# Performance work log

Measured on AMD Instinct MI355X. Metric: run time of the kernel, lower is better.

## Reference

```python
import math
import jax, jax.numpy as jnp
import numpy as np

B, D, COND, H, K, L, BOUND = 262144, 16, 8, 128, 10, 4, 1.0
D2 = math.ceil(D / 2)          # second split (spline-transformed channels) = 8
D1 = D - D2                    # passthrough channels = 8
DOUT = (3 * K + 1) * D2        # subnet output = 248
PMIN = 1e-3                    # BIN_WIDTH_MIN == BIN_HEIGHT_MIN == DELTA_MIN


def setup_inputs() -> dict:
    key = jax.random.key(0)
    ks = jax.random.split(key, 8)
    x = jax.random.normal(ks[0], (B, D), dtype=jnp.float32)
    c = jax.random.normal(ks[1], (B, COND), dtype=jnp.float32)
    din1 = D1 + COND
    W1s = jax.random.normal(ks[2], (L, din1, H), dtype=jnp.float32) * 0.1
    b1s = jnp.zeros((L, H), dtype=jnp.float32)
    Whs = jax.random.normal(ks[3], (L, H, H), dtype=jnp.float32) * 0.1
    bhs = jnp.zeros((L, H), dtype=jnp.float32)
    Wos = jax.random.normal(ks[4], (L, H, DOUT), dtype=jnp.float32) * 0.1
    bos = jnp.zeros((L, DOUT), dtype=jnp.float32)
    rng = np.random.default_rng(0)  # permutation_seed = 0
    perms = jnp.asarray(np.stack([rng.permutation(D) for _ in range(L)]), dtype=jnp.int32)
    return {"x": x, "c": c, "W1s": W1s, "b1s": b1s, "Whs": Whs, "bhs": bhs,
            "Wos": Wos, "bos": bos, "perms": perms}


def _softmax_with_min(t, m):
    return m + (1.0 - m * t.shape[-1]) * jax.nn.softmax(t, axis=-1)


def _unpack_theta(theta):
    # theta: [B, D2, 3K+1]
    bw_u, bh_u, ks_u = theta[..., :K], theta[..., K:2 * K], theta[..., 2 * K:]
    bin_w = 2.0 * BOUND * _softmax_with_min(bw_u, PMIN)
    bin_h = 2.0 * BOUND * _softmax_with_min(bh_u, PMIN)
    slopes = PMIN + (1.0 - PMIN) * jax.nn.softplus(ks_u) / math.log(2.0)
    pad = ((0, 0), (0, 0), (1, 0))
    x_knots = jnp.pad(jnp.cumsum(bin_w, axis=-1), pad) - BOUND
    y_knots = jnp.pad(jnp.cumsum(bin_h, axis=-1), pad) - BOUND
    return x_knots, y_knots, bin_w, bin_h, slopes


def _spline_fwd(x2, x_knots, y_knots, bin_w, bin_h, slopes):
    # x2: [B, D2]; knots: [B, D2, K+1]; widths/heights: [B, D2, K]; slopes: [B, D2, K+1]
    bin_idx = jnp.sum(x_knots < x2[..., None], axis=-1) - 1  # searchsorted(left) - 1
    in_bounds = (bin_idx >= 0) & (bin_idx < K)
    ci = jnp.clip(bin_idx, 0, K - 1)
    g = lambda t, i: jnp.take_along_axis(t, i[..., None], axis=-1)[..., 0]
    x1, y1 = g(x_knots, ci), g(y_knots, ci)
    xw, yw = g(bin_w, ci), g(bin_h, ci)
    d1, d2 = g(slopes, ci), g(slopes, ci + 1)
    # safe x so rational-quadratic never produces nan for masked-out lanes
    xs = jnp.where(in_bounds, x2, x1 + 0.5 * xw)
    s = yw / xw
    eta = (xs - x1) / xw
    rev_eta = 1.0 - eta
    err = eta * rev_eta
    y_denom = s + (d1 + d2 - 2.0 * s) * err
    y_rq = y1 + yw * (s * eta ** 2 + d1 * err) / y_denom
    jac_num = s ** 2 * (d2 * eta ** 2 + 2.0 * s * err + d1 * rev_eta ** 2)
    log_jac = jnp.log(jac_num) - 2.0 * jnp.log(y_denom)
    # out-of-bounds: linear extrapolation through the outermost knots
    xl, xr = x_knots[..., 0], x_knots[..., -1]
    yb, yt = y_knots[..., 0], y_knots[..., -1]
    y_lin = (yt - yb) / (xr - xl) * (x2 - xl) + yb
    yx = jnp.where(in_bounds, y_rq, y_lin)
    log_jac = jnp.where(in_bounds, log_jac, 0.0)
    return yx, jnp.sum(log_jac, axis=-1)


def _flow_forward(x, c, W1s, b1s, Whs, bhs, Wos, bos, perms):
    log_jac_det = jnp.zeros((x.shape[0],), dtype=x.dtype)
    for i in range(L):
        x1, x2 = x[:, :D1], x[:, D1:]
        h = jax.nn.relu(jnp.concatenate([x1, c], axis=1) @ W1s[i] + b1s[i])
        h = jax.nn.relu(h @ Whs[i] + bhs[i])
        theta = (h @ Wos[i] + bos[i]).reshape(-1, D2, 3 * K + 1)
        x_knots, y_knots, bin_w, bin_h, slopes = _unpack_theta(theta)
        y2, ljd = _spline_fwd(x2, x_knots, y_knots, bin_w, bin_h, slopes)
        log_jac_det = log_jac_det + ljd
        x_out = jnp.concatenate([x1, y2], axis=1)
        x = jnp.take(x_out, perms[i], axis=1)  # x @ channel_perm.T
    return x, log_jac_det


def reference(x, c, W1s, b1s, Whs, bhs, Wos, bos, perms):
    return _flow_forward(x, c, W1s, b1s, Whs, bhs, Wos, bos, perms)
```

## Files before the change

kernel.cpp:

```cpp
#include <hip/hip_runtime.h>

#define B_N   262144
#define PMIN_F 0.001f
#define LOG2E 1.44269504088896340736f
#define LN2   0.69314718055994530942f

typedef _Float16 half4v __attribute__((ext_vector_type(4)));
typedef _Float16 half8  __attribute__((ext_vector_type(8)));
typedef float    floatx4 __attribute__((ext_vector_type(4)));

__device__ __forceinline__ float fexp2(float x) { return __builtin_amdgcn_exp2f(x); }
__device__ __forceinline__ float flog2(float x) { return __builtin_amdgcn_logf(x); }
__device__ __forceinline__ float frcp (float x) { return __builtin_amdgcn_rcpf(x); }

__global__ __launch_bounds__(64) void prep_kernel(
    const float* __restrict__ W1s, const float* __restrict__ b1s,
    const float* __restrict__ Whs, const float* __restrict__ Wos,
    _Float16* __restrict__ ws)
{
    const int bid   = blockIdx.x;
    const int layer = bid / 104;
    const int r     = bid % 104;
    const int lane  = threadIdx.x;
    const int kg    = lane >> 4;
    const int c     = lane & 15;

    half8 v;
    if (r < 8) {
        const int nt = r, n = nt * 16 + c;
        const float* W1 = W1s + layer * 16 * 128;
        const float* b1 = b1s + layer * 128;
        #pragma unroll
        for (int j = 0; j < 8; ++j) {
            const int k = kg * 8 + j;
            v[j] = (k < 16) ? (_Float16)W1[k * 128 + n]
                 : (k == 16) ? (_Float16)b1[n] : (_Float16)0.f;
        }
    } else if (r < 40) {
        const int f = r - 8, nt = f >> 2, ks = f & 3, n = nt * 16 + c;
        const float* Wh = Whs + layer * 128 * 128;
        #pragma unroll
        for (int j = 0; j < 8; ++j) {
            const int k = ks * 32 + kg * 8 + j;
            v[j] = (_Float16)Wh[k * 128 + n];
        }
    } else {
        const int f = r - 40, nt = f >> 2, ks = f & 3, n = nt * 16 + c;
        const int dd = n >> 5, cc = n & 31;
        const float* Wo = Wos + layer * 128 * 248;
        #pragma unroll
        for (int j = 0; j < 8; ++j) {
            const int k = ks * 32 + kg * 8 + j;
            v[j] = (cc < 31) ? (_Float16)Wo[k * 248 + dd * 31 + cc] : (_Float16)0.f;
        }
    }
    *(half8*)(ws + (size_t)bid * 512 + lane * 8) = v;
}

__global__ __launch_bounds__(64) void flow_mfma(
    const float* __restrict__ x_in,
    const float* __restrict__ c_in,
    const float* __restrict__ bhs,
    const float* __restrict__ bos,
    const int*   __restrict__ perms,
    const _Float16* __restrict__ wsW,
    float* __restrict__ out)
{
    __shared__ __align__(16) float    xls[2][256];
    __shared__ __align__(16) _Float16 cls[2][128];
    __shared__ __align__(16) _Float16 R[2][4224];

    const int lane = threadIdx.x;
    const int q    = lane >> 4;
    const int m    = lane & 15;
    const long long row0 = (long long)blockIdx.x * 32;

    {
        const float4* xp = (const float4*)(x_in + row0 * 16);
        *(float4*)&xls[0][lane * 4] = xp[lane];
        *(float4*)&xls[1][lane * 4] = xp[lane + 64];
        const float2* cp = (const float2*)(c_in + row0 * 8);
        const float2 c0 = cp[lane], c1 = cp[lane + 64];
        cls[0][lane * 2]     = (_Float16)c0.x;
        cls[0][lane * 2 + 1] = (_Float16)c0.y;
        cls[1][lane * 2]     = (_Float16)c1.x;
        cls[1][lane * 2 + 1] = (_Float16)c1.y;
    }
    __syncthreads();

    float ljacc[4] = {0.f, 0.f, 0.f, 0.f};

    for (int l = 0; l < 4; ++l) {
        const _Float16* wsl = wsW + (size_t)l * 104 * 512;
        const float* bh = bhs + l * 128;
        const float* bo = bos + l * 248;

        half8 a1[2];
        #pragma unroll
        for (int t2 = 0; t2 < 2; ++t2) {
            #pragma unroll
            for (int j = 0; j < 8; ++j) a1[t2][j] = (_Float16)0.f;
            if (q == 0) {
                const float4 lo = *(const float4*)&xls[t2][m * 16];
                const float4 hi = *(const float4*)&xls[t2][m * 16 + 4];
                a1[t2][0] = (_Float16)lo.x; a1[t2][1] = (_Float16)lo.y;
                a1[t2][2] = (_Float16)lo.z; a1[t2][3] = (_Float16)lo.w;
                a1[t2][4] = (_Float16)hi.x; a1[t2][5] = (_Float16)hi.y;
                a1[t2][6] = (_Float16)hi.z; a1[t2][7] = (_Float16)hi.w;
            } else if (q == 1) {
                a1[t2] = *(const half8*)&cls[t2][m * 8];
            } else if (q == 2) {
                a1[t2][0] = (_Float16)1.f;
            }
        }
        {
            const floatx4 z = {0.f, 0.f, 0.f, 0.f};
            floatx4 acc0[8], acc1[8];
            #pragma unroll
            for (int nt = 0; nt < 8; ++nt) {
                const half8 b = *(const half8*)(wsl + nt * 512 + lane * 8);
                acc0[nt] = __builtin_amdgcn_mfma_f32_16x16x32_f16(a1[0], b, z, 0, 0, 0);
                acc1[nt] = __builtin_amdgcn_mfma_f32_16x16x32_f16(a1[1], b, z, 0, 0, 0);
            }
            #pragma unroll
            for (int nt = 0; nt < 8; ++nt)
                #pragma unroll
                for (int reg = 0; reg < 4; ++reg) {
                    R[0][(q * 4 + reg) * 132 + nt * 16 + m] = (_Float16)fmaxf(acc0[nt][reg], 0.f);
                    R[1][(q * 4 + reg) * 132 + nt * 16 + m] = (_Float16)fmaxf(acc1[nt][reg], 0.f);
                }
        }
        __syncthreads();

        {
            floatx4 acc0[8], acc1[8];
            #pragma unroll
            for (int nt = 0; nt < 8; ++nt) {
                const float bb = bh[nt * 16 + m];
                acc0[nt][0] = bb; acc0[nt][1] = bb; acc0[nt][2] = bb; acc0[nt][3] = bb;
                acc1[nt] = acc0[nt];
            }
            #pragma unroll
            for (int ks = 0; ks < 4; ++ks) {
                half8 a[2];
                #pragma unroll
                for (int t2 = 0; t2 < 2; ++t2) {
                    const half4v lo = *(const half4v*)&R[t2][m * 132 + ks * 32 + q * 8];
                    const half4v hi = *(const half4v*)&R[t2][m * 132 + ks * 32 + q * 8 + 4];
                    a[t2] = __builtin_shufflevector(lo, hi, 0, 1, 2, 3, 4, 5, 6, 7);
                }
                #pragma unroll
                for (int nt = 0; nt < 8; ++nt) {
                    const half8 b = *(const half8*)(wsl + (8 + nt * 4 + ks) * 512 + lane * 8);
                    acc0[nt] = __builtin_amdgcn_mfma_f32_16x16x32_f16(a[0], b, acc0[nt], 0, 0, 0);
                    acc1[nt] = __builtin_amdgcn_mfma_f32_16x16x32_f16(a[1], b, acc1[nt], 0, 0, 0);
                }
            }
            #pragma unroll
            for (int nt = 0; nt < 8; ++nt)
                #pragma unroll
                for (int reg = 0; reg < 4; ++reg) {
                    R[0][2112 + (q * 4 + reg) * 132 + nt * 16 + m] = (_Float16)fmaxf(acc0[nt][reg], 0.f);
                    R[1][2112 + (q * 4 + reg) * 132 + nt * 16 + m] = (_Float16)fmaxf(acc1[nt][reg], 0.f);
                }
        }
        __syncthreads();

        half8 a3[2][4];
        #pragma unroll
        for (int t2 = 0; t2 < 2; ++t2)
            #pragma unroll
            for (int ks = 0; ks < 4; ++ks) {
                const half4v lo = *(const half4v*)&R[t2][2112 + m * 132 + ks * 32 + q * 8];
                const half4v hi = *(const half4v*)&R[t2][2112 + m * 132 + ks * 32 + q * 8 + 4];
                a3[t2][ks] = __builtin_shufflevector(lo, hi, 0, 1, 2, 3, 4, 5, 6, 7);
            }
        __syncthreads();

        #pragma unroll
        for (int hf = 0; hf < 2; ++hf) {
            floatx4 acc0[8], acc1[8];
            #pragma unroll
            for (int nt8 = 0; nt8 < 8; ++nt8) {
                const int nt = hf * 8 + nt8;
                const float bb = ((nt & 1) && m == 15) ? 0.f
                               : bo[(nt >> 1) * 31 + (nt & 1) * 16 + m];
                acc0[nt8][0] = bb; acc0[nt8][1] = bb; acc0[nt8][2] = bb; acc0[nt8][3] = bb;
                acc1[nt8] = acc0[nt8];
            }
            #pragma unroll
            for (int ks = 0; ks < 4; ++ks) {
                #pragma unroll
                for (int nt8 = 0; nt8 < 8; ++nt8) {
                    const int nt = hf * 8 + nt8;
                    const half8 b = *(const half8*)(wsl + (40 + nt * 4 + ks) * 512 + lane * 8);
                    acc0[nt8] = __builtin_amdgcn_mfma_f32_16x16x32_f16(a3[0][ks], b, acc0[nt8], 0, 0, 0);
                    acc1[nt8] = __builtin_amdgcn_mfma_f32_16x16x32_f16(a3[1][ks], b, acc1[nt8], 0, 0, 0);
                }
            }
            #pragma unroll
            for (int nt8 = 0; nt8 < 8; ++nt8)
                #pragma unroll
                for (int reg = 0; reg < 4; ++reg) {
                    R[0][(q * 4 + reg) * 260 + (hf * 8 + nt8) * 16 + m] = (_Float16)acc0[nt8][reg];
                    R[1][(q * 4 + reg) * 260 + (hf * 8 + nt8) * 16 + m] = (_Float16)acc1[nt8][reg];
                }
        }
        __syncthreads();

        #pragma unroll
        for (int it = 0; it < 4; ++it) {
            const int t2   = it >> 1;
            const int item = lane + (it & 1) * 64;
            const int row  = item >> 3;
            const int d    = item & 7;
            const int base = row * 260 + d * 32;

            float th[31];
            #pragma unroll
            for (int j = 0; j < 8; ++j) {
                const half4v v = *(const half4v*)&R[t2][base + j * 4];
                #pragma unroll
                for (int e = 0; e < 4; ++e) {
                    const int idx = j * 4 + e;
                    if (idx < 31) th[idx] = (float)v[e];
                }
            }
            const float x2 = xls[t2][row * 16 + 8 + d];

            float bw[10], bhh[10];
            float m1 = th[0];
            #pragma unroll
            for (int i = 1; i < 10; ++i) m1 = fmaxf(m1, th[i]);
            float se = 0.f;
            #pragma unroll
            for (int i = 0; i < 10; ++i) { bw[i] = fexp2((th[i] - m1) * LOG2E); se += bw[i]; }
            const float inv = frcp(se);
            #pragma unroll
            for (int i = 0; i < 10; ++i) bw[i] = 2.f * (PMIN_F + 0.99f * bw[i] * inv);

            float m2 = th[10];
            #pragma unroll
            for (int i = 1; i < 10; ++i) m2 = fmaxf(m2, th[10 + i]);
            float se2 = 0.f;
            #pragma unroll
            for (int i = 0; i < 10; ++i) { bhh[i] = fexp2((th[10 + i] - m2) * LOG2E); se2 += bhh[i]; }
            const float inv2 = frcp(se2);
            #pragma unroll
            for (int i = 0; i < 10; ++i) bhh[i] = 2.f * (PMIN_F + 0.99f * bhh[i] * inv2);

            int cnt = (-1.f < x2) ? 1 : 0;
            float run = -1.f;
            #pragma unroll
            for (int i = 0; i < 10; ++i) { run += bw[i]; cnt += (run < x2) ? 1 : 0; }
            const int bidx = cnt - 1;
            const bool inb = (bidx >= 0) && (bidx < 10);
            const int ci = bidx < 0 ? 0 : (bidx > 9 ? 9 : bidx);

            float x1k = -1.f, y1k = -1.f, xw = 1.f, yw = 1.f, u1 = 0.f, u2 = 0.f;
            float rx = -1.f, ry = -1.f;
            #pragma unroll
            for (int i = 0; i < 10; ++i) {
                const bool pick = (i == ci);
                x1k = pick ? rx        : x1k;
                y1k = pick ? ry        : y1k;
                xw  = pick ? bw[i]     : xw;
                yw  = pick ? bhh[i]    : yw;
                u1  = pick ? th[20+i]  : u1;
                u2  = pick ? th[21+i]  : u2;
                rx += bw[i];
                ry += bhh[i];
            }
            const float t1 = u1 * LOG2E;
            const float t2s = u2 * LOG2E;
            const float dd1 = PMIN_F + 0.999f * ((t1  > 15.f) ? t1  : flog2(1.f + fexp2(t1)));
            const float dd2 = PMIN_F + 0.999f * ((t2s > 15.f) ? t2s : flog2(1.f + fexp2(t2s)));

            const float xs  = inb ? x2 : (x1k + 0.5f * xw);
            const float rxw = frcp(xw);
            const float s   = yw * rxw;
            const float eta = (xs - x1k) * rxw;
            const float rev = 1.f - eta;
            const float er  = eta * rev;
            const float dn  = s + (dd1 + dd2 - 2.f * s) * er;
            const float yrq = y1k + yw * (s * eta * eta + dd1 * er) * frcp(dn);
            const float jn  = s * s * (dd2 * eta * eta + 2.f * s * er + dd1 * rev * rev);
            const float ljx = LN2 * (flog2(jn) - 2.f * flog2(dn));
            const float ylin = (ry + 1.f) * frcp(rx + 1.f) * (x2 + 1.f) - 1.f;

            xls[t2][row * 16 + 8 + d] = inb ? yrq : ylin;

            float lj = inb ? ljx : 0.f;
            lj += __shfl_xor(lj, 1);
            lj += __shfl_xor(lj, 2);
            lj += __shfl_xor(lj, 4);
            ljacc[it] += lj;
        }
        __syncthreads();

        {
            const int4 pv = ((const int4*)(perms + l * 16))[lane & 3];
            const int mm = lane >> 2;
            const float a0 = xls[0][mm * 16 + pv.x];
            const float a1v = xls[0][mm * 16 + pv.y];
            const float a2 = xls[0][mm * 16 + pv.z];
            const float a3v = xls[0][mm * 16 + pv.w];
            const float b0 = xls[1][mm * 16 + pv.x];
            const float b1v = xls[1][mm * 16 + pv.y];
            const float b2 = xls[1][mm * 16 + pv.z];
            const float b3 = xls[1][mm * 16 + pv.w];
            __syncthreads();
            *(float4*)&xls[0][lane * 4] = make_float4(a0, a1v, a2, a3v);
            *(float4*)&xls[1][lane * 4] = make_float4(b0, b1v, b2, b3);
        }
        __syncthreads();
    }

    #pragma unroll
    for (int t2 = 0; t2 < 2; ++t2) {
        const float4 vo = *(const float4*)&xls[t2][lane * 4];
        ((float4*)(out + (row0 + t2 * 16) * 16))[lane] = vo;
    }
    #pragma unroll
    for (int t2 = 0; t2 < 2; ++t2) {
        const float a = __shfl(ljacc[t2 * 2 + 0], (lane & 7) * 8);
        const float b = __shfl(ljacc[t2 * 2 + 1], (lane & 7) * 8);
        if (lane < 16)
            out[(size_t)B_N * 16 + row0 + t2 * 16 + lane] = (lane < 8) ? a : b;
    }
}

extern "C" void kernel_launch(void* const* d_in, const int* in_sizes, int n_in,
                              void* d_out, int out_size, void* d_ws, size_t ws_size,
                              hipStream_t stream) {
    const float* x     = (const float*)d_in[0];
    const float* c     = (const float*)d_in[1];
    const float* W1s   = (const float*)d_in[2];
    const float* b1s   = (const float*)d_in[3];
    const float* Whs   = (const float*)d_in[4];
    const float* bhs   = (const float*)d_in[5];
    const float* Wos   = (const float*)d_in[6];
    const float* bos   = (const float*)d_in[7];
    const int*   perms = (const int*)d_in[8];
    float* out = (float*)d_out;
    _Float16* ws = (_Float16*)d_ws;

    prep_kernel<<<dim3(416), dim3(64), 0, stream>>>(W1s, b1s, Whs, Wos, ws);
    flow_mfma<<<dim3(B_N / 32), dim3(64), 0, stream>>>(
        x, c, bhs, bos, perms, ws, out);
}
```

Before: 318.2 us.

## Halve shared scratch and interleave spline eval per output half to raise occupancy

Cuts the R shared buffer in half by reusing one region for every layer stage. The output GEMM now writes one half (4 channels) at a time and the spline for those channels runs right after, so the full 248-column theta tile is never staged at once. The spline code is restructured to build cumulative knot arrays, pick only the bin edges, and read the two slope parameters straight from LDS, which avoids keeping a 31-float array in registers. A launch-bounds hint of 4 waves per EU is added, and the extra barriers plus the register cap could cause spills.

```diff
diff --git a/kernel.cpp b/kernel.cpp
--- a/kernel.cpp
+++ b/kernel.cpp
@@ -57,7 +57,7 @@
     *(half8*)(ws + (size_t)bid * 512 + lane * 8) = v;
 }
 
-__global__ __launch_bounds__(64) void flow_mfma(
+__global__ __launch_bounds__(64, 4) void flow_mfma(
     const float* __restrict__ x_in,
     const float* __restrict__ c_in,
     const float* __restrict__ bhs,
@@ -68,7 +68,7 @@
 {
     __shared__ __align__(16) float    xls[2][256];
     __shared__ __align__(16) _Float16 cls[2][128];
-    __shared__ __align__(16) _Float16 R[2][4224];
+    __shared__ __align__(16) _Float16 R[2][2112];
 
     const int lane = threadIdx.x;
     const int q    = lane >> 4;
@@ -88,7 +88,7 @@
     }
     __syncthreads();
 
-    float ljacc[4] = {0.f, 0.f, 0.f, 0.f};
+    float ljrow[2] = {0.f, 0.f};
 
     for (int l = 0; l < 4; ++l) {
         const _Float16* wsl = wsW + (size_t)l * 104 * 512;
@@ -132,6 +132,16 @@
         }
         __syncthreads();
 
+        half8 a2[2][4];
+        #pragma unroll
+        for (int t2 = 0; t2 < 2; ++t2)
+            #pragma unroll
+            for (int ks = 0; ks < 4; ++ks) {
+                const half4v lo = *(const half4v*)&R[t2][m * 132 + ks * 32 + q * 8];
+                const half4v hi = *(const half4v*)&R[t2][m * 132 + ks * 32 + q * 8 + 4];
+                a2[t2][ks] = __builtin_shufflevector(lo, hi, 0, 1, 2, 3, 4, 5, 6, 7);
+            }
+        __syncthreads();
         {
             floatx4 acc0[8], acc1[8];
             #pragma unroll
@@ -141,27 +151,19 @@
                 acc1[nt] = acc0[nt];
             }
             #pragma unroll
-            for (int ks = 0; ks < 4; ++ks) {
-                half8 a[2];
-                #pragma unroll
-                for (int t2 = 0; t2 < 2; ++t2) {
-                    const half4v lo = *(const half4v*)&R[t2][m * 132 + ks * 32 + q * 8];
-                    const half4v hi = *(const half4v*)&R[t2][m * 132 + ks * 32 + q * 8 + 4];
-                    a[t2] = __builtin_shufflevector(lo, hi, 0, 1, 2, 3, 4, 5, 6, 7);
-                }
+            for (int ks = 0; ks < 4; ++ks)
                 #pragma unroll
                 for (int nt = 0; nt < 8; ++nt) {
                     const half8 b = *(const half8*)(wsl + (8 + nt * 4 + ks) * 512 + lane * 8);
-                    acc0[nt] = __builtin_amdgcn_mfma_f32_16x16x32_f16(a[0], b, acc0[nt], 0, 0, 0);
-                    acc1[nt] = __builtin_amdgcn_mfma_f32_16x16x32_f16(a[1], b, acc1[nt], 0, 0, 0);
-                }
-            }
+                    acc0[nt] = __builtin_amdgcn_mfma_f32_16x16x32_f16(a2[0][ks], b, acc0[nt], 0, 0, 0);
+                    acc1[nt] = __builtin_amdgcn_mfma_f32_16x16x32_f16(a2[1][ks], b, acc1[nt], 0, 0, 0);
+                }
             #pragma unroll
             for (int nt = 0; nt < 8; ++nt)
                 #pragma unroll
                 for (int reg = 0; reg < 4; ++reg) {
-                    R[0][2112 + (q * 4 + reg) * 132 + nt * 16 + m] = (_Float16)fmaxf(acc0[nt][reg], 0.f);
-                    R[1][2112 + (q * 4 + reg) * 132 + nt * 16 + m] = (_Float16)fmaxf(acc1[nt][reg], 0.f);
+                    R[0][(q * 4 + reg) * 132 + nt * 16 + m] = (_Float16)fmaxf(acc0[nt][reg], 0.f);
+                    R[1][(q * 4 + reg) * 132 + nt * 16 + m] = (_Float16)fmaxf(acc1[nt][reg], 0.f);
                 }
         }
         __syncthreads();
@@ -171,146 +173,163 @@
         for (int t2 = 0; t2 < 2; ++t2)
             #pragma unroll
             for (int ks = 0; ks < 4; ++ks) {
-                const half4v lo = *(const half4v*)&R[t2][2112 + m * 132 + ks * 32 + q * 8];
-                const half4v hi = *(const half4v*)&R[t2][2112 + m * 132 + ks * 32 + q * 8 + 4];
+                const half4v lo = *(const half4v*)&R[t2][m * 132 + ks * 32 + q * 8];
+                const half4v hi = *(const half4v*)&R[t2][m * 132 + ks * 32 + q * 8 + 4];
                 a3[t2][ks] = __builtin_shufflevector(lo, hi, 0, 1, 2, 3, 4, 5, 6, 7);
             }
         __syncthreads();
 
         #pragma unroll
         for (int hf = 0; hf < 2; ++hf) {
-            floatx4 acc0[8], acc1[8];
-            #pragma unroll
-            for (int nt8 = 0; nt8 < 8; ++nt8) {
-                const int nt = hf * 8 + nt8;
-                const float bb = ((nt & 1) && m == 15) ? 0.f
-                               : bo[(nt >> 1) * 31 + (nt & 1) * 16 + m];
-                acc0[nt8][0] = bb; acc0[nt8][1] = bb; acc0[nt8][2] = bb; acc0[nt8][3] = bb;
-                acc1[nt8] = acc0[nt8];
-            }
-            #pragma unroll
-            for (int ks = 0; ks < 4; ++ks) {
+            {
+                floatx4 acc0[8], acc1[8];
                 #pragma unroll
                 for (int nt8 = 0; nt8 < 8; ++nt8) {
                     const int nt = hf * 8 + nt8;
-                    const half8 b = *(const half8*)(wsl + (40 + nt * 4 + ks) * 512 + lane * 8);
-                    acc0[nt8] = __builtin_amdgcn_mfma_f32_16x16x32_f16(a3[0][ks], b, acc0[nt8], 0, 0, 0);
-                    acc1[nt8] = __builtin_amdgcn_mfma_f32_16x16x32_f16(a3[1][ks], b, acc1[nt8], 0, 0, 0);
-                }
-            }
-            #pragma unroll
-            for (int nt8 = 0; nt8 < 8; ++nt8)
-                #pragma unroll
-                for (int reg = 0; reg < 4; ++reg) {
-                    R[0][(q * 4 + reg) * 260 + (hf * 8 + nt8) * 16 + m] = (_Float16)acc0[nt8][reg];
-                    R[1][(q * 4 + reg) * 260 + (hf * 8 + nt8) * 16 + m] = (_Float16)acc1[nt8][reg];
-                }
-        }
-        __syncthreads();
-
-        #pragma unroll
-        for (int it = 0; it < 4; ++it) {
-            const int t2   = it >> 1;
-            const int item = lane + (it & 1) * 64;
-            const int row  = item >> 3;
-            const int d    = item & 7;
-            const int base = row * 260 + d * 32;
-
-            float th[31];
-            #pragma unroll
-            for (int j = 0; j < 8; ++j) {
-                const half4v v = *(const half4v*)&R[t2][base + j * 4];
-                #pragma unroll
-                for (int e = 0; e < 4; ++e) {
-                    const int idx = j * 4 + e;
-                    if (idx < 31) th[idx] = (float)v[e];
-                }
-            }
-            const float x2 = xls[t2][row * 16 + 8 + d];
-
-            float bw[10], bhh[10];
-            float m1 = th[0];
-            #pragma unroll
-            for (int i = 1; i < 10; ++i) m1 = fmaxf(m1, th[i]);
-            float se = 0.f;
-            #pragma unroll
-            for (int i = 0; i < 10; ++i) { bw[i] = fexp2((th[i] - m1) * LOG2E); se += bw[i]; }
-            const float inv = frcp(se);
-            #pragma unroll
-            for (int i = 0; i < 10; ++i) bw[i] = 2.f * (PMIN_F + 0.99f * bw[i] * inv);
-
-            float m2 = th[10];
-            #pragma unroll
-            for (int i = 1; i < 10; ++i) m2 = fmaxf(m2, th[10 + i]);
-            float se2 = 0.f;
-            #pragma unroll
-            for (int i = 0; i < 10; ++i) { bhh[i] = fexp2((th[10 + i] - m2) * LOG2E); se2 += bhh[i]; }
-            const float inv2 = frcp(se2);
-            #pragma unroll
-            for (int i = 0; i < 10; ++i) bhh[i] = 2.f * (PMIN_F + 0.99f * bhh[i] * inv2);
-
-            int cnt = (-1.f < x2) ? 1 : 0;
-            float run = -1.f;
-            #pragma unroll
-            for (int i = 0; i < 10; ++i) { run += bw[i]; cnt += (run < x2) ? 1 : 0; }
-            const int bidx = cnt - 1;
-            const bool inb = (bidx >= 0) && (bidx < 10);
-            const int ci = bidx < 0 ? 0 : (bidx > 9 ? 9 : bidx);
-
-            float x1k = -1.f, y1k = -1.f, xw = 1.f, yw = 1.f, u1 = 0.f, u2 = 0.f;
-            float rx = -1.f, ry = -1.f;
-            #pragma unroll
-            for (int i = 0; i < 10; ++i) {
-                const bool pick = (i == ci);
-                x1k = pick ? rx        : x1k;
-                y1k = pick ? ry        : y1k;
-                xw  = pick ? bw[i]     : xw;
-                yw  = pick ? bhh[i]    : yw;
-                u1  = pick ? th[20+i]  : u1;
-                u2  = pick ? th[21+i]  : u2;
-                rx += bw[i];
-                ry += bhh[i];
-            }
-            const float t1 = u1 * LOG2E;
-            const float t2s = u2 * LOG2E;
-            const float dd1 = PMIN_F + 0.999f * ((t1  > 15.f) ? t1  : flog2(1.f + fexp2(t1)));
-            const float dd2 = PMIN_F + 0.999f * ((t2s > 15.f) ? t2s : flog2(1.f + fexp2(t2s)));
-
-            const float xs  = inb ? x2 : (x1k + 0.5f * xw);
-            const float rxw = frcp(xw);
-            const float s   = yw * rxw;
-            const float eta = (xs - x1k) * rxw;
-            const float rev = 1.f - eta;
-            const float er  = eta * rev;
-            const float dn  = s + (dd1 + dd2 - 2.f * s) * er;
-            const float yrq = y1k + yw * (s * eta * eta + dd1 * er) * frcp(dn);
-            const float jn  = s * s * (dd2 * eta * eta + 2.f * s * er + dd1 * rev * rev);
-            const float ljx = LN2 * (flog2(jn) - 2.f * flog2(dn));
-            const float ylin = (ry + 1.f) * frcp(rx + 1.f) * (x2 + 1.f) - 1.f;
-
-            xls[t2][row * 16 + 8 + d] = inb ? yrq : ylin;
-
-            float lj = inb ? ljx : 0.f;
-            lj += __shfl_xor(lj, 1);
-            lj += __shfl_xor(lj, 2);
-            lj += __shfl_xor(lj, 4);
-            ljacc[it] += lj;
-        }
-        __syncthreads();
+                    const float bb = ((nt & 1) && m == 15) ? 0.f
+                                   : bo[(nt >> 1) * 31 + (nt & 1) * 16 + m];
+                    acc0[nt8][0] = bb; acc0[nt8][1] = bb; acc0[nt8][2] = bb; acc0[nt8][3] = bb;
+                    acc1[nt8] = acc0[nt8];
+                }
+                #pragma unroll
+                for (int ks = 0; ks < 4; ++ks)
+                    #pragma unroll
+                    for (int nt8 = 0; nt8 < 8; ++nt8) {
+                        const int nt = hf * 8 + nt8;
+                        const half8 b = *(const half8*)(wsl + (40 + nt * 4 + ks) * 512 + lane * 8);
+                        acc0[nt8] = __builtin_amdgcn_mfma_f32_16x16x32_f16(a3[0][ks], b, acc0[nt8], 0, 0, 0);
+                        acc1[nt8] = __builtin_amdgcn_mfma_f32_16x16x32_f16(a3[1][ks], b, acc1[nt8], 0, 0, 0);
+                    }
+                #pragma unroll
+                for (int nt8 = 0; nt8 < 8; ++nt8)
+                    #pragma unroll
+                    for (int reg = 0; reg < 4; ++reg) {
+                        R[0][(q * 4 + reg) * 132 + nt8 * 16 + m] = (_Float16)acc0[nt8][reg];
+                        R[1][(q * 4 + reg) * 132 + nt8 * 16 + m] = (_Float16)acc1[nt8][reg];
+                    }
+            }
+            __syncthreads();
+
+            #pragma unroll
+            for (int itp = 0; itp < 2; ++itp) {
+                const int t2   = itp;
+                const int row  = lane >> 2;
+                const int dloc = lane & 3;
+                const int d    = hf * 4 + dloc;
+                const int base = row * 132 + dloc * 32;
+
+                const half4v v0 = *(const half4v*)&R[t2][base];
+                const half4v v1 = *(const half4v*)&R[t2][base + 4];
+                const half4v v2 = *(const half4v*)&R[t2][base + 8];
+                const half4v v3 = *(const half4v*)&R[t2][base + 12];
+                const half4v v4 = *(const half4v*)&R[t2][base + 16];
+                const float x2 = xls[t2][row * 16 + 8 + d];
+
+                float tw[10];
+                tw[0]=(float)v0[0]; tw[1]=(float)v0[1]; tw[2]=(float)v0[2]; tw[3]=(float)v0[3];
+                tw[4]=(float)v1[0]; tw[5]=(float)v1[1]; tw[6]=(float)v1[2]; tw[7]=(float)v1[3];
+                tw[8]=(float)v2[0]; tw[9]=(float)v2[1];
+
+                float cx[11], cy[11];
+                {
+                    float m1 = tw[0];
+                    #pragma unroll
+                    for (int i = 1; i < 10; ++i) m1 = fmaxf(m1, tw[i]);
+                    float se = 0.f;
+                    #pragma unroll
+                    for (int i = 0; i < 10; ++i) { tw[i] = fexp2((tw[i] - m1) * LOG2E); se += tw[i]; }
+                    const float inv198 = 1.98f * frcp(se);
+                    cx[0] = -1.f;
+                    #pragma unroll
+                    for (int i = 0; i < 10; ++i) cx[i + 1] = cx[i] + fmaf(tw[i], inv198, 0.002f);
+                }
+                {
+                    float t0=(float)v2[2], t1=(float)v2[3];
+                    float t2v=(float)v3[0], t3=(float)v3[1], t4=(float)v3[2], t5=(float)v3[3];
+                    float t6=(float)v4[0], t7=(float)v4[1], t8=(float)v4[2], t9=(float)v4[3];
+                    float hm = fmaxf(fmaxf(fmaxf(t0,t1),fmaxf(t2v,t3)),
+                                     fmaxf(fmaxf(t4,t5),fmaxf(fmaxf(t6,t7),fmaxf(t8,t9))));
+                    float e0=fexp2((t0-hm)*LOG2E), e1=fexp2((t1-hm)*LOG2E);
+                    float e2=fexp2((t2v-hm)*LOG2E), e3=fexp2((t3-hm)*LOG2E);
+                    float e4=fexp2((t4-hm)*LOG2E), e5=fexp2((t5-hm)*LOG2E);
+                    float e6=fexp2((t6-hm)*LOG2E), e7=fexp2((t7-hm)*LOG2E);
+                    float e8=fexp2((t8-hm)*LOG2E), e9=fexp2((t9-hm)*LOG2E);
+                    const float se = ((e0+e1)+(e2+e3))+((e4+e5)+((e6+e7)+(e8+e9)));
+                    const float inv198 = 1.98f * frcp(se);
+                    cy[0] = -1.f;
+                    cy[1] = cy[0] + fmaf(e0, inv198, 0.002f);
+                    cy[2] = cy[1] + fmaf(e1, inv198, 0.002f);
+                    cy[3] = cy[2] + fmaf(e2, inv198, 0.002f);
+                    cy[4] = cy[3] + fmaf(e3, inv198, 0.002f);
+                    cy[5] = cy[4] + fmaf(e4, inv198, 0.002f);
+                    cy[6] = cy[5] + fmaf(e5, inv198, 0.002f);
+                    cy[7] = cy[6] + fmaf(e6, inv198, 0.002f);
+                    cy[8] = cy[7] + fmaf(e7, inv198, 0.002f);
+                    cy[9] = cy[8] + fmaf(e8, inv198, 0.002f);
+                    cy[10]= cy[9] + fmaf(e9, inv198, 0.002f);
+                }
+
+                int cnt = 0;
+                #pragma unroll
+                for (int i = 0; i < 11; ++i) cnt += (cx[i] < x2) ? 1 : 0;
+                const int bidx = cnt - 1;
+                const bool inb = (bidx >= 0) && (bidx < 10);
+                const int ci = bidx < 0 ? 0 : (bidx > 9 ? 9 : bidx);
+
+                float xlo = cx[0], xhi = cx[1], ylo = cy[0], yhi = cy[1];
+                #pragma unroll
+                for (int i = 1; i < 10; ++i) {
+                    const bool pick = (i == ci);
+                    xlo = pick ? cx[i]     : xlo;
+                    xhi = pick ? cx[i + 1] : xhi;
+                    ylo = pick ? cy[i]     : ylo;
+                    yhi = pick ? cy[i + 1] : yhi;
+                }
+                const float xw = xhi - xlo, yw = yhi - ylo;
+                const float rx = cx[10], ry = cy[10];
+
+                const float u1 = (float)R[t2][base + 20 + ci];
+                const float u2 = (float)R[t2][base + 21 + ci];
+                const float t1 = u1 * LOG2E;
+                const float t2s = u2 * LOG2E;
+                const float dd1 = PMIN_F + 0.999f * ((t1  > 15.f) ? t1  : flog2(1.f + fexp2(t1)));
+                const float dd2 = PMIN_F + 0.999f * ((t2s > 15.f) ? t2s : flog2(1.f + fexp2(t2s)));
+
+                const float xs  = inb ? x2 : (xlo + 0.5f * xw);
+                const float rxw = frcp(xw);
+                const float s   = yw * rxw;
+                const float eta = (xs - xlo) * rxw;
+                const float rev = 1.f - eta;
+                const float er  = eta * rev;
+                const float dn  = s + (dd1 + dd2 - 2.f * s) * er;
+                const float yrq = ylo + yw * (s * eta * eta + dd1 * er) * frcp(dn);
+                const float jn  = s * s * (dd2 * eta * eta + 2.f * s * er + dd1 * rev * rev);
+                const float ljx = LN2 * (flog2(jn) - 2.f * flog2(dn));
+                const float ylin = (ry + 1.f) * frcp(rx + 1.f) * (x2 + 1.f) - 1.f;
+
+                xls[t2][row * 16 + 8 + d] = inb ? yrq : ylin;
+
+                float lj = inb ? ljx : 0.f;
+                lj += __shfl_xor(lj, 1);
+                lj += __shfl_xor(lj, 2);
+                ljrow[t2] += lj;
+            }
+            __syncthreads();
+        }
 
         {
             const int4 pv = ((const int4*)(perms + l * 16))[lane & 3];
             const int mm = lane >> 2;
             const float a0 = xls[0][mm * 16 + pv.x];
             const float a1v = xls[0][mm * 16 + pv.y];
-            const float a2 = xls[0][mm * 16 + pv.z];
+            const float a2v = xls[0][mm * 16 + pv.z];
             const float a3v = xls[0][mm * 16 + pv.w];
             const float b0 = xls[1][mm * 16 + pv.x];
             const float b1v = xls[1][mm * 16 + pv.y];
             const float b2 = xls[1][mm * 16 + pv.z];
             const float b3 = xls[1][mm * 16 + pv.w];
             __syncthreads();
-            *(float4*)&xls[0][lane * 4] = make_float4(a0, a1v, a2, a3v);
+            *(float4*)&xls[0][lane * 4] = make_float4(a0, a1v, a2v, a3v);
             *(float4*)&xls[1][lane * 4] = make_float4(b0, b1v, b2, b3);
         }
         __syncthreads();
@@ -323,10 +342,9 @@
     }
     #pragma unroll
     for (int t2 = 0; t2 < 2; ++t2) {
-        const float a = __shfl(ljacc[t2 * 2 + 0], (lane & 7) * 8);
-        const float b = __shfl(ljacc[t2 * 2 + 1], (lane & 7) * 8);
+        const float v = __shfl(ljrow[t2], (lane & 15) * 4);
         if (lane < 16)
-            out[(size_t)B_N * 16 + row0 + t2 * 16 + lane] = (lane < 8) ? a : b;
+            out[(size_t)B_N * 16 + row0 + t2 * 16 + lane] = v;
     }
 }
 
```

Measured after the change: 534.6 us. 68.0% more time.
